# Kernel optimization log

Hardware: AMD Instinct MI355X
Metric: run time of the kernel (lower is better)

## Reference

```python
import jax, jax.numpy as jnp
import numpy as np

D_MODEL, N_HEADS, N_GROUPS, BASE = 2048, 32, 8, 10000
HEAD_DIM = D_MODEL // N_HEADS  # 64


def _rope_cache(seq, head_dim, base=BASE):
    half = head_dim // 2
    theta = 1.0 / (base ** (jnp.arange(0, head_dim, 2)[:half].astype(jnp.float32) / head_dim))
    ang = jnp.einsum('i,j->ij', jnp.arange(seq, dtype=jnp.float32), theta)  # (seq, half)
    return jnp.cos(ang), jnp.sin(ang)


def _apply_rope(x):
    # x: (b, s, h, head_dim) -> interleaved-pair rotation, matching torch module
    b, s, h, hd = x.shape
    cos, sin = _rope_cache(s, hd)
    xr = x.reshape(b, s, h, hd // 2, 2)
    c = cos[None, :, None, :]
    sn = sin[None, :, None, :]
    x0, x1 = xr[..., 0], xr[..., 1]
    out = jnp.stack((x0 * c - x1 * sn, x1 * c + x0 * sn), axis=-1)
    return out.reshape(b, s, h, hd).astype(x.dtype)


def setup_inputs() -> dict:
    key = jax.random.key(0)
    ks = jax.random.split(key, 8)
    B, S = 1, 2048
    kv_dim = HEAD_DIM * N_GROUPS
    return {
        'Q': jax.random.normal(ks[0], (B, S, D_MODEL), jnp.float32),
        'K': jax.random.normal(ks[1], (B, S, D_MODEL), jnp.float32),
        'V': jax.random.normal(ks[2], (B, S, D_MODEL), jnp.float32),
        'attention_mask': jnp.ones((B, S), jnp.int32),
        'Wq': jax.random.normal(ks[3], (D_MODEL, D_MODEL), jnp.float32) * 0.02,
        'Wk': jax.random.normal(ks[4], (D_MODEL, kv_dim), jnp.float32) * 0.02,
        'Wv': jax.random.normal(ks[5], (D_MODEL, kv_dim), jnp.float32) * 0.02,
        'Wo': jax.random.normal(ks[6], (D_MODEL, D_MODEL), jnp.float32) * 0.02,
        'bo': jnp.zeros((D_MODEL,), jnp.float32),
    }


def reference(Q, K, V, attention_mask, Wq, Wk, Wv, Wo, bo):
    b, s, _ = Q.shape
    g, hpg, hd = N_GROUPS, N_HEADS // N_GROUPS, HEAD_DIM
    # projections (weights stored as [in, out], equivalent to torch x @ W.T)
    q = (Q @ Wq).reshape(b, s, N_HEADS, hd)
    q = _apply_rope(q).reshape(b, s, g, hpg, hd)
    k = _apply_rope((K @ Wk).reshape(b, s, g, hd))
    v = (V @ Wv).reshape(b, s, g, hd)

    scale = jnp.sqrt(jnp.float32(hd))
    scores = jnp.einsum('bnghd,bmgd->bnghm', q, k) / scale  # (b, s, g, hpg, s)
    # padding mask (b, 1, 1, 1, s) and causal mask (1, s, 1, 1, s)
    pad = (attention_mask != 0)[:, None, None, None, :]
    causal = jnp.tril(jnp.ones((s, s), bool))[None, :, None, None, :]
    scores = jnp.where(pad & causal, scores, -jnp.inf)
    attn = jax.nn.softmax(scores, axis=-1)  # dropout p=0.0 -> identity
    out = jnp.einsum('bnghm,bmgd->bnghd', attn, v).reshape(b, s, D_MODEL)
    return out @ Wo + bo
```

## Files before the change

kernel.cpp:

```cpp
#include <hip/hip_runtime.h>

typedef __bf16 bf16_t;
typedef __bf16 bf16x8 __attribute__((ext_vector_type(8)));
typedef __bf16 bf16x4 __attribute__((ext_vector_type(4)));
typedef __bf16 bf16x2 __attribute__((ext_vector_type(2)));
typedef float  f32x4  __attribute__((ext_vector_type(4)));

#define LOG2E 1.44269504088896340736f

#define GLDS(gp, lp)                                                           \
  __builtin_amdgcn_global_load_lds(                                            \
      (const __attribute__((address_space(1))) void*)(gp),                     \
      (__attribute__((address_space(3))) void*)(lp), 16, 0, 0)

__global__ __launch_bounds__(256) void rope_table_k(float* __restrict__ cs,
                                                    float* __restrict__ sn, int S) {
  int i = blockIdx.x * 256 + threadIdx.x;
  if (i >= S * 32) return;
  int s = i >> 5, j = i & 31;
  float theta = powf(10000.0f, -(float)j * (1.0f / 32.0f));
  float a = (float)s * theta;
  cs[i] = cosf(a);
  sn[i] = sinf(a);
}

__global__ __launch_bounds__(256) void cast3_k(const float* __restrict__ A,
                                               const float* __restrict__ B,
                                               const float* __restrict__ C,
                                               bf16_t* __restrict__ oa,
                                               bf16_t* __restrict__ ob,
                                               bf16_t* __restrict__ oc) {
  const int b = blockIdx.x;
  const float* in; bf16_t* out;
  if (b < 2048) { in = A; out = oa; }
  else if (b < 4096) { in = B; out = ob; }
  else { in = C; out = oc; }
  const int j = (b & 2047) * 256 + threadIdx.x;
  const float4 v0 = *(const float4*)&in[(size_t)j * 8];
  const float4 v1 = *(const float4*)&in[(size_t)j * 8 + 4];
  bf16x8 o;
  o[0]=(bf16_t)v0.x; o[1]=(bf16_t)v0.y; o[2]=(bf16_t)v0.z; o[3]=(bf16_t)v0.w;
  o[4]=(bf16_t)v1.x; o[5]=(bf16_t)v1.y; o[6]=(bf16_t)v1.z; o[7]=(bf16_t)v1.w;
  *(bf16x8*)&out[(size_t)j * 8] = o;
}

__global__ void transpose4_k(const float* __restrict__ Wq, const float* __restrict__ Wk,
                             const float* __restrict__ Wv, const float* __restrict__ Wo,
                             bf16_t* __restrict__ WqT, bf16_t* __restrict__ WkT,
                             bf16_t* __restrict__ WvT, bf16_t* __restrict__ WoT) {
  __shared__ float tile[32][33];
  const int bx = blockIdx.x;
  const float* in; bf16_t* out; int C, cbl;
  if (bx < 64)      { in = Wq; out = WqT; C = 2048; cbl = bx; }
  else if (bx < 80) { in = Wk; out = WkT; C = 512;  cbl = bx - 64; }
  else if (bx < 96) { in = Wv; out = WvT; C = 512;  cbl = bx - 80; }
  else              { in = Wo; out = WoT; C = 2048; cbl = bx - 96; }
  const int R = 2048;
  int c0 = cbl * 32, r0 = blockIdx.y * 32;
  int tx = threadIdx.x, ty = threadIdx.y;
  #pragma unroll
  for (int k = 0; k < 32; k += 8)
    tile[ty + k][tx] = in[(size_t)(r0 + ty + k) * C + c0 + tx];
  __syncthreads();
  #pragma unroll
  for (int k = 0; k < 32; k += 8)
    out[(size_t)(c0 + ty + k) * R + r0 + tx] = (bf16_t)tile[tx][ty + k];
}

__device__ __forceinline__ int xcd_swz(int bid, int nb) {
  const int q = nb >> 3;
  return (bid & 7) * q + (bid >> 3);
}
__device__ __forceinline__ void st_map(int lin, int nstc, int& rb, int& cb) {
  const int stid = lin >> 4, w = lin & 15;
  const int sr = stid / nstc, t = stid - sr * nstc;
  const int sc = (sr & 1) ? (nstc - 1 - t) : t;
  rb = sr * 4 + (w >> 2);
  cb = sc * 4 + (w & 3);
}

template<int MODE>
__global__ __launch_bounds__(256) void gemm_glds_k(
    const bf16_t* __restrict__ Aq, const bf16_t* __restrict__ Ak, const bf16_t* __restrict__ Av,
    const bf16_t* __restrict__ Bq, const bf16_t* __restrict__ Bk, const bf16_t* __restrict__ Bv,
    const int K, const float* __restrict__ cs, const float* __restrict__ sn,
    bf16_t* __restrict__ oq, bf16_t* __restrict__ okg, bf16_t* __restrict__ ovt,
    float* __restrict__ ofp, const float* __restrict__ bias, const int S) {
  constexpr int BN   = (MODE == 0) ? 128 : 64;
  constexpr int NI   = BN / 32;
  constexpr int BU   = BN / 32;
  constexpr int NB   = (MODE == 0) ? 768 : 1024;
  constexpr int NSTC = (MODE == 0) ? 6 : 8;
  __shared__ bf16_t a_lds[64 * 64];
  __shared__ bf16_t b_lds[BN * 64];
  const int tid = threadIdx.x, wid = tid >> 6, lane = tid & 63;
  const int fr = lane & 15, kg = lane >> 4;

  const int lin = xcd_swz(blockIdx.x, NB);
  int rb, cb; st_map(lin, NSTC, rb, cb);
  const bf16_t* Ap; const bf16_t* Bp; int emode, col0;
  if (MODE == 1)    { Ap = Aq; Bp = Bq; emode = 3; col0 = cb * BN; }
  else if (cb < 16) { Ap = Aq; Bp = Bq; emode = 0; col0 = cb * 128; }
  else if (cb < 20) { Ap = Ak; Bp = Bk; emode = 1; col0 = (cb - 16) * 128; }
  else              { Ap = Av; Bp = Bv; emode = 2; col0 = (cb - 20) * 128; }
  const int row0 = rb * 64;
  const int wr = (wid >> 1) * 32, wc = (wid & 1) * (BN / 2);

  f32x4 acc[2][NI];
  #pragma unroll
  for (int i = 0; i < 2; ++i)
    #pragma unroll
    for (int j = 0; j < NI; ++j)
      acc[i][j] = (f32x4){0.f, 0.f, 0.f, 0.f};

  const int rloc = lane >> 3;
  const int schunk = ((lane & 7) ^ rloc) * 8;
  const bf16_t* gA0 = Ap + (size_t)(row0 + (wid * 2 + 0) * 8 + rloc) * K + schunk;
  const bf16_t* gA1 = Ap + (size_t)(row0 + (wid * 2 + 1) * 8 + rloc) * K + schunk;
  bf16_t* lA0 = &a_lds[(wid * 2 + 0) * 512];
  bf16_t* lA1 = &a_lds[(wid * 2 + 1) * 512];
  const bf16_t* gB[BU];
  bf16_t* lB[BU];
  #pragma unroll
  for (int u = 0; u < BU; ++u) {
    gB[u] = Bp + (size_t)(col0 + (wid * BU + u) * 8 + rloc) * K + schunk;
    lB[u] = &b_lds[(wid * BU + u) * 512];
  }

  for (int kt = 0; kt < K; kt += 64) {
    __syncthreads();
    GLDS(gA0 + kt, lA0);
    GLDS(gA1 + kt, lA1);
    #pragma unroll
    for (int u = 0; u < BU; ++u) GLDS(gB[u] + kt, lB[u]);
    __syncthreads();
    #pragma unroll
    for (int ks = 0; ks < 2; ++ks) {
      bf16x8 af[2], bfr[NI];
      #pragma unroll
      for (int mi = 0; mi < 2; ++mi) {
        const int r = wr + mi * 16 + fr;
        af[mi] = *(const bf16x8*)&a_lds[r * 64 + (((ks * 4 + kg) ^ (fr & 7)) * 8)];
      }
      #pragma unroll
      for (int ni = 0; ni < NI; ++ni) {
        const int r = wc + ni * 16 + fr;
        bfr[ni] = *(const bf16x8*)&b_lds[r * 64 + (((ks * 4 + kg) ^ (fr & 7)) * 8)];
      }
      #pragma unroll
      for (int mi = 0; mi < 2; ++mi)
        #pragma unroll
        for (int ni = 0; ni < NI; ++ni)
          acc[mi][ni] = __builtin_amdgcn_mfma_f32_16x16x32_bf16(af[mi], bfr[ni], acc[mi][ni], 0, 0, 0);
    }
  }

  #pragma unroll
  for (int mi = 0; mi < 2; ++mi) {
    #pragma unroll
    for (int ni = 0; ni < NI; ++ni) {
      #pragma unroll
      for (int r = 0; r < 4; ++r) {
        const int grow = row0 + wr + mi * 16 + kg * 4 + r;
        const int gcol = col0 + wc + ni * 16 + fr;
        float v = acc[mi][ni][r];
        if (emode == 3) {
          ofp[(size_t)grow * 2048 + gcol] = v + bias[gcol];
        } else if (emode == 2) {
          const int gi = gcol >> 6, d = gcol & 63;
          ovt[((size_t)gi * 64 + d) * S + grow] = (bf16_t)v;
        } else {
          const float pv = __shfl_xor(v, 1);
          const int d = gcol & 63, p = d >> 1, hh = gcol >> 6;
          const float c = cs[grow * 32 + p], s = sn[grow * 32 + p];
          float o = (d & 1) ? fmaf(pv, s, v * c) : fmaf(-pv, s, v * c);
          if (emode == 0) {
            o *= 0.125f * LOG2E;
            oq[((size_t)hh * S + grow) * 64 + d] = (bf16_t)o;
          } else {
            okg[((size_t)hh * S + grow) * 64 + d] = (bf16_t)o;
          }
        }
      }
    }
  }
}

__device__ __forceinline__ int swz8(int r, int c) { return r * 64 + (((c) ^ (r & 7)) << 3); }

__global__ __launch_bounds__(256) void attn_k(
    const bf16_t* __restrict__ qh,
    const bf16_t* __restrict__ kgr,
    const bf16_t* __restrict__ vtg,
    const int* __restrict__ amask,
    bf16_t* __restrict__ ao,
    const int S) {
  __shared__ bf16_t k_lds[64 * 64];
  __shared__ bf16_t vt_lds[64 * 64];
  __shared__ bf16_t p_lds[4][16 * 64];
  const int tid = threadIdx.x, wid = tid >> 6, lane = tid & 63;
  const int fr = lane & 15, kgp = lane >> 4;
  const int h = blockIdx.x, g = h >> 2;
  const int qb = 31 - blockIdx.y;
  const int q0 = qb * 64 + wid * 16;
  const int qg = q0 + fr;

  const bf16_t* qbase = qh + ((size_t)h * S + q0 + fr) * 64;
  const bf16x8 qf0 = *(const bf16x8*)&qbase[kgp * 8];
  const bf16x8 qf1 = *(const bf16x8*)&qbase[32 + kgp * 8];

  f32x4 oacc[4];
  #pragma unroll
  for (int t = 0; t < 4; ++t) oacc[t] = (f32x4){0.f, 0.f, 0.f, 0.f};
  float m_ = -1e30f, l_ = 0.f;

  const int srow = tid >> 2, sc4 = tid & 3;
  const bf16_t* kbase = kgr + (size_t)g * S * 64;
  const bf16_t* vbase = vtg + (size_t)g * 64 * S;
  const int cmax = qb + 1;

  bf16x8 nk0 = *(const bf16x8*)&kbase[(size_t)srow * 64 + sc4 * 8];
  bf16x8 nk1 = *(const bf16x8*)&kbase[(size_t)srow * 64 + 32 + sc4 * 8];
  bf16x8 nv0 = *(const bf16x8*)&vbase[(size_t)srow * S + sc4 * 8];
  bf16x8 nv1 = *(const bf16x8*)&vbase[(size_t)srow * S + 32 + sc4 * 8];
  int mvc = amask[lane];
  *(bf16x8*)&k_lds[swz8(srow, sc4)]      = nk0;
  *(bf16x8*)&k_lds[swz8(srow, 4 + sc4)]  = nk1;
  *(bf16x8*)&vt_lds[swz8(srow, sc4)]     = nv0;
  *(bf16x8*)&vt_lds[swz8(srow, 4 + sc4)] = nv1;
  __syncthreads();

  for (int c = 0; c < cmax; ++c) {
    const int kc0 = c * 64;
    const unsigned long long pm = __ballot(mvc == 0);
    const bool more = (c + 1 < cmax);
    if (more) {
      const int kc1 = kc0 + 64;
      nk0 = *(const bf16x8*)&kbase[(size_t)(kc1 + srow) * 64 + sc4 * 8];
      nk1 = *(const bf16x8*)&kbase[(size_t)(kc1 + srow) * 64 + 32 + sc4 * 8];
      nv0 = *(const bf16x8*)&vbase[(size_t)srow * S + kc1 + sc4 * 8];
      nv1 = *(const bf16x8*)&vbase[(size_t)srow * S + kc1 + 32 + sc4 * 8];
      mvc = amask[kc1 + lane];
    }

    f32x4 sc[4];
    #pragma unroll
    for (int a = 0; a < 4; ++a) {
      const bf16x8 ka0 = *(const bf16x8*)&k_lds[swz8(a * 16 + fr, kgp)];
      const bf16x8 ka1 = *(const bf16x8*)&k_lds[swz8(a * 16 + fr, 4 + kgp)];
      f32x4 z = (f32x4){0.f, 0.f, 0.f, 0.f};
      z = __builtin_amdgcn_mfma_f32_16x16x32_bf16(ka0, qf0, z, 0, 0, 0);
      z = __builtin_amdgcn_mfma_f32_16x16x32_bf16(ka1, qf1, z, 0, 0, 0);
      sc[a] = z;
    }

    if (c == qb) {
      #pragma unroll
      for (int a = 0; a < 4; ++a)
        #pragma unroll
        for (int r = 0; r < 4; ++r) {
          const int kl = a * 16 + 4 * kgp + r;
          if (kc0 + kl > qg) sc[a][r] = -1e30f;
        }
    }
    if (pm) {
      #pragma unroll
      for (int a = 0; a < 4; ++a)
        #pragma unroll
        for (int r = 0; r < 4; ++r) {
          const int kl = a * 16 + 4 * kgp + r;
          if ((pm >> kl) & 1) sc[a][r] = -1e30f;
        }
    }

    float t0 = fmaxf(fmaxf(sc[0][0], sc[0][1]), fmaxf(sc[0][2], sc[0][3]));
    float t1 = fmaxf(fmaxf(sc[1][0], sc[1][1]), fmaxf(sc[1][2], sc[1][3]));
    float t2 = fmaxf(fmaxf(sc[2][0], sc[2][1]), fmaxf(sc[2][2], sc[2][3]));
    float t3 = fmaxf(fmaxf(sc[3][0], sc[3][1]), fmaxf(sc[3][2], sc[3][3]));
    float smax = fmaxf(fmaxf(t0, t1), fmaxf(t2, t3));
    smax = fmaxf(smax, __shfl_xor(smax, 16));
    smax = fmaxf(smax, __shfl_xor(smax, 32));

    const bool rescale = !__all(smax <= m_ + 8.0f);
    if (rescale) {
      const float mn = fmaxf(m_, smax);
      const float al = exp2f(m_ - mn);
      m_ = mn;
      #pragma unroll
      for (int t = 0; t < 4; ++t)
        #pragma unroll
        for (int r = 0; r < 4; ++r) oacc[t][r] *= al;
      l_ *= al;
    }

    float ps = 0.f;
    #pragma unroll
    for (int a = 0; a < 4; ++a)
      #pragma unroll
      for (int r = 0; r < 4; ++r) {
        const float p = exp2f(sc[a][r] - m_);
        sc[a][r] = p;
        ps += p;
      }
    ps += __shfl_xor(ps, 16);
    ps += __shfl_xor(ps, 32);
    l_ += ps;

    #pragma unroll
    for (int a = 0; a < 4; ++a) {
      bf16x4 w;
      w[0] = (bf16_t)sc[a][0];
      w[1] = (bf16_t)sc[a][1];
      w[2] = (bf16_t)sc[a][2];
      w[3] = (bf16_t)sc[a][3];
      const int off = a * 16 + 4 * kgp;
      *(bf16x4*)&p_lds[wid][fr * 64 + (((off >> 3) ^ (fr & 7)) << 3) + (off & 7)] = w;
    }
    const bf16x8 pa0 = *(const bf16x8*)&p_lds[wid][swz8(fr, kgp)];
    const bf16x8 pa1 = *(const bf16x8*)&p_lds[wid][swz8(fr, 4 + kgp)];

    #pragma unroll
    for (int t = 0; t < 4; ++t) {
      const bf16x8 vb0 = *(const bf16x8*)&vt_lds[swz8(t * 16 + fr, kgp)];
      const bf16x8 vb1 = *(const bf16x8*)&vt_lds[swz8(t * 16 + fr, 4 + kgp)];
      oacc[t] = __builtin_amdgcn_mfma_f32_16x16x32_bf16(vb0, pa0, oacc[t], 0, 0, 0);
      oacc[t] = __builtin_amdgcn_mfma_f32_16x16x32_bf16(vb1, pa1, oacc[t], 0, 0, 0);
    }

    if (more) {
      __syncthreads();
      *(bf16x8*)&k_lds[swz8(srow, sc4)]      = nk0;
      *(bf16x8*)&k_lds[swz8(srow, 4 + sc4)]  = nk1;
      *(bf16x8*)&vt_lds[swz8(srow, sc4)]     = nv0;
      *(bf16x8*)&vt_lds[swz8(srow, 4 + sc4)] = nv1;
      __syncthreads();
    }
  }

  const float inv = 1.0f / l_;
  #pragma unroll
  for (int t = 0; t < 4; ++t) {
    bf16x4 o4;
    #pragma unroll
    for (int r = 0; r < 4; ++r) o4[r] = (bf16_t)(oacc[t][r] * inv);
    *(bf16x4*)&ao[(size_t)(q0 + fr) * 2048 + h * 64 + t * 16 + 4 * kgp] = o4;
  }
}

extern "C" void kernel_launch(void* const* d_in, const int* in_sizes, int n_in,
                              void* d_out, int out_size, void* d_ws, size_t ws_size,
                              hipStream_t stream) {
  const float* Q  = (const float*)d_in[0];
  const float* K  = (const float*)d_in[1];
  const float* V  = (const float*)d_in[2];
  const int*   am = (const int*)d_in[3];
  const float* Wq = (const float*)d_in[4];
  const float* Wk = (const float*)d_in[5];
  const float* Wv = (const float*)d_in[6];
  const float* Wo = (const float*)d_in[7];
  const float* bo = (const float*)d_in[8];
  float* out = (float*)d_out;

  const int S = 2048, D = 2048;
  char* w = (char*)d_ws;
  const size_t MB = 1u << 20;
  bf16_t* WqT = (bf16_t*)(w + 0 * MB);
  bf16_t* WoT = (bf16_t*)(w + 8 * MB);
  bf16_t* WkT = (bf16_t*)(w + 16 * MB);
  bf16_t* WvT = (bf16_t*)(w + 18 * MB);
  bf16_t* qh  = (bf16_t*)(w + 20 * MB);
  bf16_t* kgr = (bf16_t*)(w + 28 * MB);
  bf16_t* vtg = (bf16_t*)(w + 30 * MB);
  bf16_t* ao  = (bf16_t*)(w + 32 * MB);
  bf16_t* Qb  = (bf16_t*)(w + 40 * MB);
  bf16_t* Kb  = (bf16_t*)(w + 48 * MB);
  bf16_t* Vb  = (bf16_t*)(w + 56 * MB);
  float*  cs  = (float*)(w + 64 * MB);
  float*  sn  = (float*)(w + 64 * MB + 256 * 1024);

  rope_table_k<<<256, 256, 0, stream>>>(cs, sn, S);
  cast3_k<<<6144, 256, 0, stream>>>(Q, K, V, Qb, Kb, Vb);
  transpose4_k<<<dim3(160, 64), dim3(32, 8), 0, stream>>>(Wq, Wk, Wv, Wo, WqT, WkT, WvT, WoT);

  gemm_glds_k<0><<<768, 256, 0, stream>>>(Qb, Kb, Vb, WqT, WkT, WvT, D,
                                          cs, sn, qh, kgr, vtg, nullptr, nullptr, S);

  attn_k<<<dim3(32, 32), 256, 0, stream>>>(qh, kgr, vtg, am, ao, S);

  gemm_glds_k<1><<<1024, 256, 0, stream>>>(ao, nullptr, nullptr, WoT, nullptr, nullptr,
                                           D, nullptr, nullptr, nullptr, nullptr, nullptr,
                                           out, bo, S);
}
```

Measured before the change: 149.9 us.

## Fuse fp32-to-bf16 activation cast into QKV projection GEMM A-tile loads

Removes the separate cast kernel that converted Q, K, V to bf16. The QKV GEMM now loads the fp32 activations straight into registers, converts them to bf16, and writes them into swizzled LDS, prefetching the next k-tile into registers while the current one is computed. This drops a kernel launch and a bf16 write-then-read round trip. In exchange the GEMM reads twice as many A bytes, and the A path goes through registers instead of direct global-to-LDS loads, which adds VGPR pressure. Since every A tile is reused by several column blocks, the extra fp32 traffic repeats across them.

After: 142.9 us. 4.7% less time.

```diff
diff --git a/kernel.cpp b/kernel.cpp
--- a/kernel.cpp
+++ b/kernel.cpp
@@ -22,26 +22,6 @@
   float a = (float)s * theta;
   cs[i] = cosf(a);
   sn[i] = sinf(a);
-}
-
-__global__ __launch_bounds__(256) void cast3_k(const float* __restrict__ A,
-                                               const float* __restrict__ B,
-                                               const float* __restrict__ C,
-                                               bf16_t* __restrict__ oa,
-                                               bf16_t* __restrict__ ob,
-                                               bf16_t* __restrict__ oc) {
-  const int b = blockIdx.x;
-  const float* in; bf16_t* out;
-  if (b < 2048) { in = A; out = oa; }
-  else if (b < 4096) { in = B; out = ob; }
-  else { in = C; out = oc; }
-  const int j = (b & 2047) * 256 + threadIdx.x;
-  const float4 v0 = *(const float4*)&in[(size_t)j * 8];
-  const float4 v1 = *(const float4*)&in[(size_t)j * 8 + 4];
-  bf16x8 o;
-  o[0]=(bf16_t)v0.x; o[1]=(bf16_t)v0.y; o[2]=(bf16_t)v0.z; o[3]=(bf16_t)v0.w;
-  o[4]=(bf16_t)v1.x; o[5]=(bf16_t)v1.y; o[6]=(bf16_t)v1.z; o[7]=(bf16_t)v1.w;
-  *(bf16x8*)&out[(size_t)j * 8] = o;
 }
 
 __global__ void transpose4_k(const float* __restrict__ Wq, const float* __restrict__ Wk,
@@ -81,7 +61,7 @@
 
 template<int MODE>
 __global__ __launch_bounds__(256) void gemm_glds_k(
-    const bf16_t* __restrict__ Aq, const bf16_t* __restrict__ Ak, const bf16_t* __restrict__ Av,
+    const void* __restrict__ Aq, const void* __restrict__ Ak, const void* __restrict__ Av,
     const bf16_t* __restrict__ Bq, const bf16_t* __restrict__ Bk, const bf16_t* __restrict__ Bv,
     const int K, const float* __restrict__ cs, const float* __restrict__ sn,
     bf16_t* __restrict__ oq, bf16_t* __restrict__ okg, bf16_t* __restrict__ ovt,
@@ -98,7 +78,7 @@
 
   const int lin = xcd_swz(blockIdx.x, NB);
   int rb, cb; st_map(lin, NSTC, rb, cb);
-  const bf16_t* Ap; const bf16_t* Bp; int emode, col0;
+  const void* Ap; const bf16_t* Bp; int emode, col0;
   if (MODE == 1)    { Ap = Aq; Bp = Bq; emode = 3; col0 = cb * BN; }
   else if (cb < 16) { Ap = Aq; Bp = Bq; emode = 0; col0 = cb * 128; }
   else if (cb < 20) { Ap = Ak; Bp = Bk; emode = 1; col0 = (cb - 16) * 128; }
@@ -115,10 +95,6 @@
 
   const int rloc = lane >> 3;
   const int schunk = ((lane & 7) ^ rloc) * 8;
-  const bf16_t* gA0 = Ap + (size_t)(row0 + (wid * 2 + 0) * 8 + rloc) * K + schunk;
-  const bf16_t* gA1 = Ap + (size_t)(row0 + (wid * 2 + 1) * 8 + rloc) * K + schunk;
-  bf16_t* lA0 = &a_lds[(wid * 2 + 0) * 512];
-  bf16_t* lA1 = &a_lds[(wid * 2 + 1) * 512];
   const bf16_t* gB[BU];
   bf16_t* lB[BU];
   #pragma unroll
@@ -127,13 +103,47 @@
     lB[u] = &b_lds[(wid * BU + u) * 512];
   }
 
+  const bf16_t* gA0 = nullptr; const bf16_t* gA1 = nullptr;
+  bf16_t *lA0 = nullptr, *lA1 = nullptr;
+  const float* Afp = (const float*)Ap;
+  int arow = 0, acol = 0;
+  f32x4 ar0, ar1, ar2, ar3;
+  if (MODE == 1) {
+    gA0 = (const bf16_t*)Ap + (size_t)(row0 + (wid * 2 + 0) * 8 + rloc) * K + schunk;
+    gA1 = (const bf16_t*)Ap + (size_t)(row0 + (wid * 2 + 1) * 8 + rloc) * K + schunk;
+    lA0 = &a_lds[(wid * 2 + 0) * 512];
+    lA1 = &a_lds[(wid * 2 + 1) * 512];
+  } else {
+    arow = wid * 16 + (lane >> 2);
+    acol = (lane & 3) * 16;
+    const float* p = &Afp[(size_t)(row0 + arow) * K + acol];
+    ar0 = *(const f32x4*)(p); ar1 = *(const f32x4*)(p + 4);
+    ar2 = *(const f32x4*)(p + 8); ar3 = *(const f32x4*)(p + 12);
+  }
+
   for (int kt = 0; kt < K; kt += 64) {
     __syncthreads();
-    GLDS(gA0 + kt, lA0);
-    GLDS(gA1 + kt, lA1);
+    if (MODE == 0) {
+      bf16x8 w0, w1;
+      w0[0]=(bf16_t)ar0[0]; w0[1]=(bf16_t)ar0[1]; w0[2]=(bf16_t)ar0[2]; w0[3]=(bf16_t)ar0[3];
+      w0[4]=(bf16_t)ar1[0]; w0[5]=(bf16_t)ar1[1]; w0[6]=(bf16_t)ar1[2]; w0[7]=(bf16_t)ar1[3];
+      w1[0]=(bf16_t)ar2[0]; w1[1]=(bf16_t)ar2[1]; w1[2]=(bf16_t)ar2[2]; w1[3]=(bf16_t)ar2[3];
+      w1[4]=(bf16_t)ar3[0]; w1[5]=(bf16_t)ar3[1]; w1[6]=(bf16_t)ar3[2]; w1[7]=(bf16_t)ar3[3];
+      const int c0w = (lane & 3) * 2;
+      *(bf16x8*)&a_lds[arow * 64 + ((c0w ^ (arow & 7)) * 8)]       = w0;
+      *(bf16x8*)&a_lds[arow * 64 + (((c0w + 1) ^ (arow & 7)) * 8)] = w1;
+    } else {
+      GLDS(gA0 + kt, lA0);
+      GLDS(gA1 + kt, lA1);
+    }
     #pragma unroll
     for (int u = 0; u < BU; ++u) GLDS(gB[u] + kt, lB[u]);
     __syncthreads();
+    if (MODE == 0 && kt + 64 < K) {
+      const float* p = &Afp[(size_t)(row0 + arow) * K + kt + 64 + acol];
+      ar0 = *(const f32x4*)(p); ar1 = *(const f32x4*)(p + 4);
+      ar2 = *(const f32x4*)(p + 8); ar3 = *(const f32x4*)(p + 12);
+    }
     #pragma unroll
     for (int ks = 0; ks < 2; ++ks) {
       bf16x8 af[2], bfr[NI];
@@ -372,17 +382,13 @@
   bf16_t* kgr = (bf16_t*)(w + 28 * MB);
   bf16_t* vtg = (bf16_t*)(w + 30 * MB);
   bf16_t* ao  = (bf16_t*)(w + 32 * MB);
-  bf16_t* Qb  = (bf16_t*)(w + 40 * MB);
-  bf16_t* Kb  = (bf16_t*)(w + 48 * MB);
-  bf16_t* Vb  = (bf16_t*)(w + 56 * MB);
-  float*  cs  = (float*)(w + 64 * MB);
-  float*  sn  = (float*)(w + 64 * MB + 256 * 1024);
+  float*  cs  = (float*)(w + 40 * MB);
+  float*  sn  = (float*)(w + 40 * MB + 256 * 1024);
 
   rope_table_k<<<256, 256, 0, stream>>>(cs, sn, S);
-  cast3_k<<<6144, 256, 0, stream>>>(Q, K, V, Qb, Kb, Vb);
   transpose4_k<<<dim3(160, 64), dim3(32, 8), 0, stream>>>(Wq, Wk, Wv, Wo, WqT, WkT, WvT, WoT);
 
-  gemm_glds_k<0><<<768, 256, 0, stream>>>(Qb, Kb, Vb, WqT, WkT, WvT, D,
+  gemm_glds_k<0><<<768, 256, 0, stream>>>(Q, K, V, WqT, WkT, WvT, D,
                                           cs, sn, qh, kgr, vtg, nullptr, nullptr, S);
 
   attn_k<<<dim3(32, 32), 256, 0, stream>>>(qh, kgr, vtg, am, ao, S);
```
